# Kernel optimization log

Measured on AMD Instinct MI355X. Metric: run time of the kernel, lower is better.

Reference implementation:

```python
import jax, jax.numpy as jnp
import numpy as np

NUM_GROUPS, GROUP_SIZE, D_MODEL = 8, 4096, 1024
NUM_EXPERTS = 64
EXPERT_CAPACITY = 1024  # capacity_factor 2: 2 * total_tokens / num_experts


def setup_inputs() -> dict:
    key = jax.random.key(0)
    k1, k2, k3 = jax.random.split(key, 3)
    x = jax.random.normal(k1, (NUM_GROUPS, GROUP_SIZE, D_MODEL), dtype=jnp.float32)
    gate_kernel = jax.random.normal(k2, (D_MODEL, NUM_EXPERTS), dtype=jnp.float32) * 0.1
    gate_bias = jax.random.normal(k3, (NUM_EXPERTS,), dtype=jnp.float32) * 0.01
    temperature = jnp.ones((1,), dtype=jnp.float32)
    return {
        "x": x,
        "gate_kernel": gate_kernel,
        "gate_bias": gate_bias,
        "temperature": temperature,
        "expert_capacity": EXPERT_CAPACITY,
    }


def reference(x, gate_kernel, gate_bias, temperature, expert_capacity):
    # x: [G, S, D]; gate_kernel: [D, E]
    G, S, _ = x.shape
    E = gate_kernel.shape[1]

    router_logits = jnp.einsum("gsd,de->gse", x, gate_kernel) + gate_bias  # [G, S, E]
    safe_temp = jnp.maximum(temperature, 0.1)  # [1]
    router_probs = jax.nn.softmax(router_logits / safe_temp, axis=-1)  # [G, S, E]

    # Per-expert top-k over all flattened tokens.
    flat_probs = router_probs.transpose(2, 0, 1).reshape(E, G * S)  # [E, G*S]
    scores, token_indices = jax.lax.top_k(flat_probs, k=expert_capacity)  # [E, C]

    group_indices = token_indices // S  # [E, C]
    pos_indices = token_indices % S  # [E, C]
    expert_ids = jnp.broadcast_to(jnp.arange(E)[:, None], scores.shape)  # [E, C]

    # use_mask_routing=True path: scatter into capacity-limited dense masks.
    expert_masks = jnp.zeros((E, G, S), dtype=jnp.bool_).at[
        expert_ids, group_indices, pos_indices].set(True)
    weight_masks = jnp.zeros((E, G, S), dtype=x.dtype).at[
        expert_ids, group_indices, pos_indices].set(scores)

    loss = jnp.asarray(0.0, dtype=x.dtype)  # training=False
    return expert_masks, weight_masks, loss
```

## Files before the change

### kernel.cpp

```cpp
#include <hip/hip_runtime.h>
#include <math.h>

#define NG 8
#define SEQ 4096
#define DM 1024
#define NE 64
#define GS (NG * SEQ)
#define KSEL 1024
#define MASK_ELEMS (NE * GS)
#define SEG 16
#define SEGLEN (GS / SEG)
#define CAP 2048
#define CAP2 16384

typedef __attribute__((ext_vector_type(8))) short short8;
typedef __attribute__((ext_vector_type(4))) float f32x4;

__device__ __forceinline__ unsigned short f2bf(float v) {
  unsigned u = __float_as_uint(v);
  return (unsigned short)((u + 0x7FFFu + ((u >> 16) & 1u)) >> 16);
}
__device__ __forceinline__ float bf2f(unsigned short h) {
  return __uint_as_float(((unsigned)h) << 16);
}

#define GLDS(gsrc, ldst)                                                             \
  __builtin_amdgcn_global_load_lds(                                                  \
      (const __attribute__((address_space(1))) void*)(gsrc),                         \
      (__attribute__((address_space(3))) void*)(ldst), 16, 0, 0)

__global__ __launch_bounds__(256)
void k_split(const float* __restrict__ w, unsigned short* __restrict__ wph,
             unsigned short* __restrict__ wpm, unsigned* __restrict__ zbase) {
  const int t = blockIdx.x * 256 + threadIdx.x;
  if (t < NE * 256 + NE) zbase[t] = 0u;
  const int k = t >> 6, e = t & 63;
  float v = w[t];
  unsigned short h = f2bf(v); float r = v - bf2f(h);
  const int tile = k >> 5, g = (k >> 3) & 3, j = k & 7;
  const int cb = e >> 4, lrow = e & 15;
  const size_t o = (size_t)(tile * 4 + cb) * 512 + (g * 16 + lrow) * 8 + j;
  wph[o] = h; wpm[o] = f2bf(r);
}

__global__ __launch_bounds__(256, 2)
void k_gemm_softmax(const float* __restrict__ x,
                    const unsigned short* __restrict__ wph,
                    const unsigned short* __restrict__ wpm,
                    const float* __restrict__ bias, const float* __restrict__ temp,
                    float* __restrict__ probsT) {
  __shared__ float S[16384];
  float (*Pt)[68] = (float (*)[68])S;

  const int tid = threadIdx.x;
  const int w = tid >> 6, lane = tid & 63;
  const int lrow = lane & 15, g = lane >> 4;
  const int m0 = blockIdx.x * 64;
  const int ks0 = blockIdx.x & 15;
  const int arow_g = tid >> 4;
  const int agr = (tid & 15) ^ (arow_g & 15);

#define TS(u) (((u) + ks0) & 15)

  int irow[4], jcol[4];
  {
    union { unsigned short u[8]; short8 v; } ar, on;
#pragma unroll
    for (int j = 0; j < 8; ++j) { ar.u[j] = f2bf((float)lrow); on.u[j] = 0x3F80u; }
    f32x4 z = {0.f, 0.f, 0.f, 0.f};
    f32x4 p1 = __builtin_amdgcn_mfma_f32_16x16x32_bf16(ar.v, on.v, z, 0, 0, 0);
    f32x4 p2 = __builtin_amdgcn_mfma_f32_16x16x32_bf16(on.v, ar.v, z, 0, 0, 0);
#pragma unroll
    for (int b = 0; b < 4; ++b) {
      irow[b] = ((int)p1[b]) >> 5;
      jcol[b] = ((int)p2[b]) >> 5;
    }
  }

  f32x4 acc[4];
#pragma unroll
  for (int cb = 0; cb < 4; ++cb) acc[cb] = (f32x4){0.f, 0.f, 0.f, 0.f};

#define ISSUE(s, buf)                                                                \
  {                                                                                  \
    _Pragma("unroll")                                                                \
    for (int c = 0; c < 4; ++c)                                                      \
      GLDS(x + (size_t)(m0 + c * 16 + arow_g) * DM + (s) * 64 + agr * 4,             \
           S + (buf) * 8192 + (c * 256 + tid) * 4);                                  \
    _Pragma("unroll")                                                                \
    for (int p = 0; p < 2; ++p)                                                      \
      _Pragma("unroll")                                                              \
      for (int c = 0; c < 2; ++c)                                                    \
        GLDS((p ? wpm : wph) + (size_t)(s) * 4096 + c * 2048 + tid * 8,              \
             S + (buf) * 8192 + 4096 + p * 2048 + c * 1024 + tid * 4);               \
  }

#define COMPUTE(buf)                                                                 \
  {                                                                                  \
    const float* Af = S + (buf) * 8192;                                              \
    const unsigned short* Bb = (const unsigned short*)(S + (buf) * 8192 + 4096);     \
    _Pragma("unroll")                                                                \
    for (int kt = 0; kt < 2; ++kt) {                                                 \
      f32x4 lo = *(const f32x4*)(Af + (w * 16 + lrow) * 64 +                         \
                                 ((kt * 8 + g * 2 + 0) ^ lrow) * 4);                 \
      f32x4 hi = *(const f32x4*)(Af + (w * 16 + lrow) * 64 +                         \
                                 ((kt * 8 + g * 2 + 1) ^ lrow) * 4);                 \
      union { unsigned short u[8]; short8 v; } ah, am;                               \
      _Pragma("unroll")                                                              \
      for (int j = 0; j < 8; ++j) {                                                  \
        float v0 = (j < 4) ? lo[j] : hi[j - 4];                                      \
        unsigned short h_ = f2bf(v0);                                                \
        ah.u[j] = h_; am.u[j] = f2bf(v0 - bf2f(h_));                                 \
      }                                                                              \
      _Pragma("unroll")                                                              \
      for (int cb = 0; cb < 4; ++cb) {                                               \
        short8 bh_ = *(const short8*)(Bb + (kt * 4 + cb) * 512 + lane * 8);          \
        short8 bm_ = *(const short8*)(Bb + 4096 + (kt * 4 + cb) * 512 + lane * 8);   \
        acc[cb] = __builtin_amdgcn_mfma_f32_16x16x32_bf16(ah.v, bh_, acc[cb], 0, 0, 0); \
        acc[cb] = __builtin_amdgcn_mfma_f32_16x16x32_bf16(am.v, bh_, acc[cb], 0, 0, 0); \
        acc[cb] = __builtin_amdgcn_mfma_f32_16x16x32_bf16(ah.v, bm_, acc[cb], 0, 0, 0); \
      }                                                                              \
    }                                                                                \
  }

#define WAIT8 { asm volatile("s_waitcnt vmcnt(8)" ::: "memory");                     \
                __builtin_amdgcn_sched_barrier(0); }
#define WAIT0 { asm volatile("s_waitcnt vmcnt(0)" ::: "memory");                     \
                __builtin_amdgcn_sched_barrier(0); }

  ISSUE(TS(0), 0);
  ISSUE(TS(1), 1);
#pragma unroll
  for (int s = 0; s < 14; ++s) {
    WAIT8;
    __builtin_amdgcn_s_barrier();
    if (s & 1) { COMPUTE(1); } else { COMPUTE(0); }
    __builtin_amdgcn_s_barrier();
    ISSUE(TS(s + 2), s & 1);
  }
  WAIT8; __builtin_amdgcn_s_barrier(); COMPUTE(0);
  __builtin_amdgcn_s_barrier();
  WAIT0; __builtin_amdgcn_s_barrier(); COMPUTE(1);
  __syncthreads();

#undef ISSUE
#undef COMPUTE
#undef WAIT8
#undef WAIT0
#undef TS

  {
    float st = temp[0];
    if (st < 0.1f) st = 0.1f;
    const float inv_t = 1.0f / st;
#pragma unroll
    for (int b = 0; b < 4; ++b) {
      float l[4];
      float mx = -1.0e30f;
#pragma unroll
      for (int cb = 0; cb < 4; ++cb) {
        l[cb] = (acc[cb][b] + bias[cb * 16 + jcol[b]]) * inv_t;
        mx = fmaxf(mx, l[cb]);
      }
      mx = fmaxf(mx, __shfl_xor(mx, 1));
      mx = fmaxf(mx, __shfl_xor(mx, 2));
      mx = fmaxf(mx, __shfl_xor(mx, 4));
      mx = fmaxf(mx, __shfl_xor(mx, 8));
      float p[4], sm = 0.0f;
#pragma unroll
      for (int cb = 0; cb < 4; ++cb) { p[cb] = __expf(l[cb] - mx); sm += p[cb]; }
      sm += __shfl_xor(sm, 1);
      sm += __shfl_xor(sm, 2);
      sm += __shfl_xor(sm, 4);
      sm += __shfl_xor(sm, 8);
      const float invs = 1.0f / sm;
#pragma unroll
      for (int cb = 0; cb < 4; ++cb)
        Pt[cb * 16 + jcol[b]][w * 16 + irow[b]] = p[cb] * invs;
    }
  }
  __syncthreads();

  {
    const int e = tid >> 2, qq = tid & 3;
    float* dst = probsT + (size_t)e * GS + m0 + qq * 16;
#pragma unroll
    for (int c2 = 0; c2 < 4; ++c2)
      *(float4*)(dst + c2 * 4) = *(const float4*)(&Pt[e][qq * 16 + c2 * 4]);
  }
}

__device__ __forceinline__ void pick_scan(const unsigned* __restrict__ bins,
                                          unsigned r_in, unsigned& bucket,
                                          unsigned& r_out, unsigned* res) {
  __syncthreads();
  const int tid = threadIdx.x;
  if (tid < 64) {
    uint4 b = ((const uint4*)bins)[tid];
    unsigned s3 = b.w, s2 = b.z + s3, s1 = b.y + s2, s0 = b.x + s1;
    unsigned suf = s0;
#pragma unroll
    for (int off = 1; off < 64; off <<= 1) {
      unsigned t = __shfl_down(suf, off);
      if (tid + off < 64) suf += t;
    }
    unsigned above = suf - s0;
    unsigned inc0 = above + s0, inc1 = above + s1, inc2 = above + s2, inc3 = above + s3;
    if (inc3 >= r_in && inc3 - b.w < r_in) { res[0] = 4 * tid + 3; res[1] = r_in - (inc3 - b.w); }
    if (inc2 >= r_in && inc2 - b.z < r_in) { res[0] = 4 * tid + 2; res[1] = r_in - (inc2 - b.z); }
    if (inc1 >= r_in && inc1 - b.y < r_in) { res[0] = 4 * tid + 1; res[1] = r_in - (inc1 - b.y); }
    if (inc0 >= r_in && inc0 - b.x < r_in) { res[0] = 4 * tid + 0; res[1] = r_in - (inc0 - b.x); }
  }
  __syncthreads();
  bucket = res[0];
  r_out = res[1];
}

__global__ __launch_bounds__(256)
void k_hist0(const float* __restrict__ probsT, unsigned* __restrict__ ghist0) {
  __shared__ unsigned h[4][256];
  const int tid = threadIdx.x, wv = tid >> 6;
  const int e = blockIdx.x >> 4;
  const int seg = blockIdx.x & (SEG - 1);
  h[0][tid] = 0; h[1][tid] = 0; h[2][tid] = 0; h[3][tid] = 0;
  __syncthreads();
  const float4* col = (const float4*)(probsT + (size_t)e * GS + seg * SEGLEN);
#pragma unroll
  for (int i = 0; i < SEGLEN / 1024; ++i) {
    float4 v = col[i * 256 + tid];
    atomicAdd(&h[wv][__float_as_uint(v.x) >> 24], 1u);
    atomicAdd(&h[wv][__float_as_uint(v.y) >> 24], 1u);
    atomicAdd(&h[wv][__float_as_uint(v.z) >> 24], 1u);
    atomicAdd(&h[wv][__float_as_uint(v.w) >> 24], 1u);
  }
  __syncthreads();
  unsigned c = h[0][tid] + h[1][tid] + h[2][tid] + h[3][tid];
  if (c) atomicAdd(&ghist0[e * 256 + tid], c);
}

__global__ __launch_bounds__(256)
void k_compact(const float* __restrict__ probsT, const unsigned* __restrict__ ghist0,
               unsigned* __restrict__ cCnt, int* __restrict__ cIdx,
               float* __restrict__ cKey) {
  __shared__ unsigned res[2];
  __shared__ unsigned locN, basePos;
  __shared__ int locIdx[2048];
  __shared__ float locKey[2048];
  const int tid = threadIdx.x;
  const int e = blockIdx.x >> 4;
  const int seg = blockIdx.x & (SEG - 1);

  if (tid == 0) locN = 0u;
  unsigned b0, r0;
  pick_scan(ghist0 + e * 256, KSEL, b0, r0, res);
  const unsigned blo = (b0 == 0u) ? 0u : (b0 - 1u);

  const float* col = probsT + (size_t)e * GS + seg * SEGLEN;
  for (int i = 0; i < SEGLEN / 256; ++i) {
    const int t = i * 256 + tid;
    const float p = col[t];
    if ((__float_as_uint(p) >> 24) >= blo) {
      unsigned pos = atomicAdd(&locN, 1u);
      locIdx[pos] = seg * SEGLEN + t;
      locKey[pos] = p;
    }
  }
  __syncthreads();
  if (tid == 0) basePos = locN ? atomicAdd(&cCnt[e], locN) : 0u;
  __syncthreads();
  const unsigned n = locN, bp = basePos;
  for (unsigned i = tid; i < n; i += 256) {
    const unsigned gp = bp + i;
    if (gp < CAP2) {
      cIdx[(size_t)e * CAP2 + gp] = locIdx[i];
      cKey[(size_t)e * CAP2 + gp] = locKey[i];
    }
  }
}

__global__ __launch_bounds__(256)
void k_select2(const unsigned* __restrict__ ghist0, const unsigned* __restrict__ cCnt,
               const int* __restrict__ cIdx, const float* __restrict__ cKey,
               const float* __restrict__ temp, unsigned* __restrict__ defCnt,
               unsigned* __restrict__ candCnt, int* __restrict__ candIdx,
               float* __restrict__ thrHiA) {
  __shared__ unsigned res[2];
  __shared__ unsigned h[4][256];
  __shared__ unsigned hs[256];
  __shared__ unsigned nd, nc;
  const int tid = threadIdx.x, wv = tid >> 6;
  const int e = blockIdx.x;
  const int cnt = (int)min(cCnt[e], (unsigned)CAP2);

  unsigned b0, r;
  pick_scan(ghist0 + e * 256, KSEL, b0, r, res);
  unsigned pfx = b0 << 24;

  for (int pass = 1; pass < 4; ++pass) {
    const int shift = 24 - 8 * pass;
    const unsigned hm = 0xFFFFFFFFu << (shift + 8);
    for (int i = tid; i < 1024; i += 256) ((unsigned*)h)[i] = 0u;
    __syncthreads();
    for (int i = tid; i < cnt; i += 256) {
      unsigned key = __float_as_uint(cKey[(size_t)e * CAP2 + i]);
      if ((key & hm) == (pfx & hm)) atomicAdd(&h[wv][(key >> shift) & 255], 1u);
    }
    __syncthreads();
    hs[tid] = h[0][tid] + h[1][tid] + h[2][tid] + h[3][tid];
    unsigned b, rn;
    pick_scan(hs, r, b, rn, res);
    pfx |= b << shift;
    r = rn;
  }

  const float thrv = __uint_as_float(pfx);
  float st = temp[0];
  if (st < 0.1f) st = 0.1f;
  const float rel = 2.0e-3f / st;
  const float hi = thrv * (1.0f + rel);
  const float lo = thrv * (1.0f - rel);
  if (tid == 0) thrHiA[e] = hi;

  if (tid == 0) { nd = 0u; nc = 0u; }
  __syncthreads();
  for (int i = tid; i < cnt; i += 256) {
    const float p = cKey[(size_t)e * CAP2 + i];
    const int t = cIdx[(size_t)e * CAP2 + i];
    if (p > hi) {
      atomicAdd(&nd, 1u);
    } else if (p >= lo) {
      unsigned pos = atomicAdd(&nc, 1u);
      if (pos < CAP) candIdx[e * CAP + pos] = t;
    }
  }
  __syncthreads();
  if (tid == 0) {
    defCnt[e] = nd;
    candCnt[e] = min(nc, (unsigned)CAP);
  }
}

__global__ __launch_bounds__(256)
void k_repair(const float* __restrict__ x, const float* __restrict__ w,
              const float* __restrict__ bias, const float* __restrict__ temp,
              const unsigned* __restrict__ candCnt, const int* __restrict__ candIdx,
              double* __restrict__ candKey) {
  __shared__ double red[4][64];
  const int e = blockIdx.x >> 4;
  const int chunk = blockIdx.x & 15;
  const int tid = threadIdx.x;
  const int ee = tid & 63, q = tid >> 6;
  const int cnt = (int)min(candCnt[e], (unsigned)CAP);

  double st = (double)temp[0];
  if (st < 0.1) st = 0.1;
  const double inv_t = 1.0 / st;

  for (int i = chunk; i < cnt; i += 16) {
    const int t = candIdx[e * CAP + i];
    const float* xr = x + (size_t)t * DM;
    double s0 = 0.0, s1 = 0.0, s2 = 0.0, s3 = 0.0;
    const int kb = q * 256;
    for (int k = kb; k < kb + 256; k += 4) {
      s0 += (double)xr[k + 0] * (double)w[(size_t)(k + 0) * NE + ee];
      s1 += (double)xr[k + 1] * (double)w[(size_t)(k + 1) * NE + ee];
      s2 += (double)xr[k + 2] * (double)w[(size_t)(k + 2) * NE + ee];
      s3 += (double)xr[k + 3] * (double)w[(size_t)(k + 3) * NE + ee];
    }
    red[q][ee] = (s0 + s1) + (s2 + s3);
    __syncthreads();
    if (tid < 64) {
      double l = (red[0][tid] + red[1][tid] + red[2][tid] + red[3][tid] +
                  (double)bias[tid]) * inv_t;
      double m = l;
#pragma unroll
      for (int off = 1; off < 64; off <<= 1) m = fmax(m, __shfl_xor(m, off));
      double ex = exp(l - m);
      double ss = ex;
#pragma unroll
      for (int off = 1; off < 64; off <<= 1) ss += __shfl_xor(ss, off);
      if (tid == e) candKey[e * CAP + i] = ex / ss;
    }
    __syncthreads();
  }
}

__global__ __launch_bounds__(256)
void k_scatter(const float* __restrict__ probsT, const float* __restrict__ thrHiA,
               float* __restrict__ out) {
  const int gid = blockIdx.x * 256 + threadIdx.x;
  const int base = gid * 4;
  const int e = base >> 15;
  float4 p = *(const float4*)(probsT + (size_t)base);
  const float hi = thrHiA[e];
  float pv[4] = {p.x, p.y, p.z, p.w};
  float mk[4], wt[4];
#pragma unroll
  for (int c = 0; c < 4; ++c) {
    bool sel = pv[c] > hi;
    mk[c] = sel ? 1.0f : 0.0f;
    wt[c] = sel ? pv[c] : 0.0f;
  }
  *(float4*)(out + (size_t)base) = make_float4(mk[0], mk[1], mk[2], mk[3]);
  *(float4*)(out + (size_t)MASK_ELEMS + base) = make_float4(wt[0], wt[1], wt[2], wt[3]);
  if (gid == 0) out[2 * (size_t)MASK_ELEMS] = 0.0f;
}

__global__ __launch_bounds__(256)
void k_finish(const unsigned* __restrict__ defCnt, const unsigned* __restrict__ candCnt,
              const int* __restrict__ candIdx, const double* __restrict__ candKey,
              const float* __restrict__ probsT, float* __restrict__ out) {
  __shared__ double kd[CAP];
  __shared__ int ti[CAP];
  const int e = blockIdx.x, tid = threadIdx.x;
  const int cnt = (int)min(candCnt[e], (unsigned)CAP);
  const int need = KSEL - (int)defCnt[e];

  for (int i = tid; i < cnt; i += 256) {
    kd[i] = candKey[e * CAP + i];
    ti[i] = candIdx[e * CAP + i];
  }
  __syncthreads();
  for (int i = tid; i < cnt; i += 256) {
    const double ki = kd[i];
    const int tii = ti[i];
    int rank = 0;
    for (int j = 0; j < cnt; ++j)
      rank += (kd[j] > ki) || (kd[j] == ki && ti[j] < tii);
    if (rank < need) {
      out[(size_t)e * GS + tii] = 1.0f;
      out[(size_t)MASK_ELEMS + (size_t)e * GS + tii] = probsT[(size_t)e * GS + tii];
    }
  }
}

extern "C" void kernel_launch(void* const* d_in, const int* in_sizes, int n_in,
                              void* d_out, int out_size, void* d_ws, size_t ws_size,
                              hipStream_t stream) {
  const float* x    = (const float*)d_in[0];
  const float* gw   = (const float*)d_in[1];
  const float* gb   = (const float*)d_in[2];
  const float* temp = (const float*)d_in[3];

  float* probsT    = (float*)d_ws;
  unsigned* ghist0 = (unsigned*)((char*)d_ws + (size_t)MASK_ELEMS * 4);
  unsigned* cCnt   = ghist0 + NE * 256;
  unsigned* defCnt = cCnt + NE;
  unsigned* candCnt = defCnt + NE;
  float* thrHiA    = (float*)(candCnt + NE);
  int* candIdx     = (int*)(thrHiA + NE);
  double* candKey  = (double*)(candIdx + NE * CAP);
  int* cIdx        = (int*)(candKey + NE * CAP);
  float* cKey      = (float*)(cIdx + (size_t)NE * CAP2);
  unsigned short* wph = (unsigned short*)(cKey + (size_t)NE * CAP2);
  unsigned short* wpm = wph + DM * NE;

  k_split<<<DM * NE / 256, 256, 0, stream>>>(gw, wph, wpm, ghist0);
  k_gemm_softmax<<<GS / 64, 256, 0, stream>>>(x, wph, wpm, gb, temp, probsT);
  k_hist0<<<NE * SEG, 256, 0, stream>>>(probsT, ghist0);
  k_compact<<<NE * SEG, 256, 0, stream>>>(probsT, ghist0, cCnt, cIdx, cKey);
  k_select2<<<NE, 256, 0, stream>>>(ghist0, cCnt, cIdx, cKey, temp, defCnt,
                                    candCnt, candIdx, thrHiA);
  k_repair<<<NE * 16, 256, 0, stream>>>(x, gw, gb, temp, candCnt, candIdx, candKey);
  k_scatter<<<MASK_ELEMS / 1024, 256, 0, stream>>>(probsT, thrHiA, (float*)d_out);
  k_finish<<<NE, 256, 0, stream>>>(defCnt, candCnt, candIdx, candKey,
                                   probsT, (float*)d_out);
}
```

Baseline: 92.47 us.

## Fuse top-byte histogram into GEMM-softmax and deepen load pipeline to four stages

Removes the separate k_hist0 kernel. The GEMM-softmax kernel now builds a per-block 64x256 top-byte histogram in shared memory and atomically adds it to the global histogram, which avoids re-reading the full probsT array. The K-loop is also restructured into 32-wide K steps with a 4-deep ring buffer and vmcnt(12) waits. This deepens the prefetch, but the waits become finer-grained. The trade-off is extra block-level work: a 16K-entry LDS zero-fill and flush loop, plus many global atomics from every one of the 512 blocks.

```diff
diff --git a/kernel.cpp b/kernel.cpp
--- a/kernel.cpp
+++ b/kernel.cpp
@@ -48,19 +48,18 @@
                     const unsigned short* __restrict__ wph,
                     const unsigned short* __restrict__ wpm,
                     const float* __restrict__ bias, const float* __restrict__ temp,
-                    float* __restrict__ probsT) {
+                    float* __restrict__ probsT, unsigned* __restrict__ ghist0) {
   __shared__ float S[16384];
+  unsigned* Su = (unsigned*)S;
   float (*Pt)[68] = (float (*)[68])S;
 
   const int tid = threadIdx.x;
   const int w = tid >> 6, lane = tid & 63;
   const int lrow = lane & 15, g = lane >> 4;
   const int m0 = blockIdx.x * 64;
-  const int ks0 = blockIdx.x & 15;
-  const int arow_g = tid >> 4;
-  const int agr = (tid & 15) ^ (arow_g & 15);
-
-#define TS(u) (((u) + ks0) & 15)
+  const int ks0 = blockIdx.x & 31;
+
+#define TS(u) (((u) + ks0) & 31)
 
   int irow[4], jcol[4];
   {
@@ -84,71 +83,72 @@
 #define ISSUE(s, buf)                                                                \
   {                                                                                  \
     _Pragma("unroll")                                                                \
-    for (int c = 0; c < 4; ++c)                                                      \
-      GLDS(x + (size_t)(m0 + c * 16 + arow_g) * DM + (s) * 64 + agr * 4,             \
-           S + (buf) * 8192 + (c * 256 + tid) * 4);                                  \
+    for (int c = 0; c < 2; ++c) {                                                    \
+      const int idx = c * 256 + tid;                                                 \
+      const int row = idx >> 3, kg = (idx & 7) ^ (row & 7);                          \
+      GLDS(x + (size_t)(m0 + row) * DM + (s) * 32 + kg * 4,                          \
+           S + (buf) * 4096 + idx * 4);                                              \
+    }                                                                                \
     _Pragma("unroll")                                                                \
-    for (int p = 0; p < 2; ++p)                                                      \
-      _Pragma("unroll")                                                              \
-      for (int c = 0; c < 2; ++c)                                                    \
-        GLDS((p ? wpm : wph) + (size_t)(s) * 4096 + c * 2048 + tid * 8,              \
-             S + (buf) * 8192 + 4096 + p * 2048 + c * 1024 + tid * 4);               \
+    for (int c = 0; c < 2; ++c) {                                                    \
+      const int idx = c * 256 + tid;                                                 \
+      const unsigned short* bp = (idx >> 8) ? wpm : wph;                             \
+      GLDS(bp + (size_t)(s) * 2048 + (idx & 255) * 8,                                \
+           S + (buf) * 4096 + 2048 + idx * 4);                                       \
+    }                                                                                \
   }
 
 #define COMPUTE(buf)                                                                 \
   {                                                                                  \
-    const float* Af = S + (buf) * 8192;                                              \
-    const unsigned short* Bb = (const unsigned short*)(S + (buf) * 8192 + 4096);     \
+    const float* Af = S + (buf) * 4096;                                              \
+    const unsigned short* Bb = (const unsigned short*)(S + (buf) * 4096 + 2048);     \
+    const int row = w * 16 + lrow;                                                   \
+    f32x4 lo = *(const f32x4*)(Af + row * 32 + ((g * 2 + 0) ^ (row & 7)) * 4);       \
+    f32x4 hi = *(const f32x4*)(Af + row * 32 + ((g * 2 + 1) ^ (row & 7)) * 4);       \
+    union { unsigned short u[8]; short8 v; } ah, am;                                 \
     _Pragma("unroll")                                                                \
-    for (int kt = 0; kt < 2; ++kt) {                                                 \
-      f32x4 lo = *(const f32x4*)(Af + (w * 16 + lrow) * 64 +                         \
-                                 ((kt * 8 + g * 2 + 0) ^ lrow) * 4);                 \
-      f32x4 hi = *(const f32x4*)(Af + (w * 16 + lrow) * 64 +                         \
-                                 ((kt * 8 + g * 2 + 1) ^ lrow) * 4);                 \
-      union { unsigned short u[8]; short8 v; } ah, am;                               \
-      _Pragma("unroll")                                                              \
-      for (int j = 0; j < 8; ++j) {                                                  \
-        float v0 = (j < 4) ? lo[j] : hi[j - 4];                                      \
-        unsigned short h_ = f2bf(v0);                                                \
-        ah.u[j] = h_; am.u[j] = f2bf(v0 - bf2f(h_));                                 \
-      }                                                                              \
-      _Pragma("unroll")                                                              \
-      for (int cb = 0; cb < 4; ++cb) {                                               \
-        short8 bh_ = *(const short8*)(Bb + (kt * 4 + cb) * 512 + lane * 8);          \
-        short8 bm_ = *(const short8*)(Bb + 4096 + (kt * 4 + cb) * 512 + lane * 8);   \
-        acc[cb] = __builtin_amdgcn_mfma_f32_16x16x32_bf16(ah.v, bh_, acc[cb], 0, 0, 0); \
-        acc[cb] = __builtin_amdgcn_mfma_f32_16x16x32_bf16(am.v, bh_, acc[cb], 0, 0, 0); \
-        acc[cb] = __builtin_amdgcn_mfma_f32_16x16x32_bf16(ah.v, bm_, acc[cb], 0, 0, 0); \
-      }                                                                              \
+    for (int j = 0; j < 8; ++j) {                                                    \
+      float v0 = (j < 4) ? lo[j] : hi[j - 4];                                        \
+      unsigned short h_ = f2bf(v0);                                                  \
+      ah.u[j] = h_; am.u[j] = f2bf(v0 - bf2f(h_));                                   \
     }                                                                                \
-  }
-
-#define WAIT8 { asm volatile("s_waitcnt vmcnt(8)" ::: "memory");                     \
-                __builtin_amdgcn_sched_barrier(0); }
-#define WAIT0 { asm volatile("s_waitcnt vmcnt(0)" ::: "memory");                     \
-                __builtin_amdgcn_sched_barrier(0); }
+    _Pragma("unroll")                                                                \
+    for (int cb = 0; cb < 4; ++cb) {                                                 \
+      short8 bh_ = *(const short8*)(Bb + cb * 512 + lane * 8);                       \
+      short8 bm_ = *(const short8*)(Bb + 2048 + cb * 512 + lane * 8);                \
+      acc[cb] = __builtin_amdgcn_mfma_f32_16x16x32_bf16(ah.v, bh_, acc[cb], 0, 0, 0);\
+      acc[cb] = __builtin_amdgcn_mfma_f32_16x16x32_bf16(am.v, bh_, acc[cb], 0, 0, 0);\
+      acc[cb] = __builtin_amdgcn_mfma_f32_16x16x32_bf16(ah.v, bm_, acc[cb], 0, 0, 0);\
+    }                                                                                \
+  }
+
+#define WAITN(n) { asm volatile("s_waitcnt vmcnt(" #n ")" ::: "memory");             \
+                   __builtin_amdgcn_sched_barrier(0); }
 
   ISSUE(TS(0), 0);
   ISSUE(TS(1), 1);
-#pragma unroll
-  for (int s = 0; s < 14; ++s) {
-    WAIT8;
+  ISSUE(TS(2), 2);
+  ISSUE(TS(3), 3);
+#pragma unroll
+  for (int s = 0; s < 28; ++s) {
+    WAITN(12);
     __builtin_amdgcn_s_barrier();
-    if (s & 1) { COMPUTE(1); } else { COMPUTE(0); }
+    COMPUTE(s & 3);
     __builtin_amdgcn_s_barrier();
-    ISSUE(TS(s + 2), s & 1);
-  }
-  WAIT8; __builtin_amdgcn_s_barrier(); COMPUTE(0);
-  __builtin_amdgcn_s_barrier();
-  WAIT0; __builtin_amdgcn_s_barrier(); COMPUTE(1);
+    ISSUE(TS(s + 4), s & 3);
+  }
+  WAITN(12); __builtin_amdgcn_s_barrier(); COMPUTE(0);
+  WAITN(8);  __builtin_amdgcn_s_barrier(); COMPUTE(1);
+  WAITN(4);  __builtin_amdgcn_s_barrier(); COMPUTE(2);
+  WAITN(0);  __builtin_amdgcn_s_barrier(); COMPUTE(3);
   __syncthreads();
 
 #undef ISSUE
 #undef COMPUTE
-#undef WAIT8
-#undef WAIT0
+#undef WAITN
 #undef TS
 
+  float pn[4][4];
   {
     float st = temp[0];
     if (st < 0.1f) st = 0.1f;
@@ -175,12 +175,32 @@
       sm += __shfl_xor(sm, 8);
       const float invs = 1.0f / sm;
 #pragma unroll
-      for (int cb = 0; cb < 4; ++cb)
-        Pt[cb * 16 + jcol[b]][w * 16 + irow[b]] = p[cb] * invs;
-    }
-  }
-  __syncthreads();
-
+      for (int cb = 0; cb < 4; ++cb) pn[b][cb] = p[cb] * invs;
+    }
+  }
+
+  for (int i = tid; i < 16384; i += 256) Su[i] = 0u;
+  __syncthreads();
+#pragma unroll
+  for (int b = 0; b < 4; ++b)
+#pragma unroll
+    for (int cb = 0; cb < 4; ++cb) {
+      const int e = cb * 16 + jcol[b];
+      atomicAdd(&Su[e * 256 + (__float_as_uint(pn[b][cb]) >> 24)], 1u);
+    }
+  __syncthreads();
+  for (int i = tid; i < 16384; i += 256) {
+    const unsigned h = Su[i];
+    if (h) atomicAdd(&ghist0[i], h);
+  }
+  __syncthreads();
+
+#pragma unroll
+  for (int b = 0; b < 4; ++b)
+#pragma unroll
+    for (int cb = 0; cb < 4; ++cb)
+      Pt[cb * 16 + jcol[b]][w * 16 + irow[b]] = pn[b][cb];
+  __syncthreads();
   {
     const int e = tid >> 2, qq = tid & 3;
     float* dst = probsT + (size_t)e * GS + m0 + qq * 16;
@@ -214,28 +234,6 @@
   __syncthreads();
   bucket = res[0];
   r_out = res[1];
-}
-
-__global__ __launch_bounds__(256)
-void k_hist0(const float* __restrict__ probsT, unsigned* __restrict__ ghist0) {
-  __shared__ unsigned h[4][256];
-  const int tid = threadIdx.x, wv = tid >> 6;
-  const int e = blockIdx.x >> 4;
-  const int seg = blockIdx.x & (SEG - 1);
-  h[0][tid] = 0; h[1][tid] = 0; h[2][tid] = 0; h[3][tid] = 0;
-  __syncthreads();
-  const float4* col = (const float4*)(probsT + (size_t)e * GS + seg * SEGLEN);
-#pragma unroll
-  for (int i = 0; i < SEGLEN / 1024; ++i) {
-    float4 v = col[i * 256 + tid];
-    atomicAdd(&h[wv][__float_as_uint(v.x) >> 24], 1u);
-    atomicAdd(&h[wv][__float_as_uint(v.y) >> 24], 1u);
-    atomicAdd(&h[wv][__float_as_uint(v.z) >> 24], 1u);
-    atomicAdd(&h[wv][__float_as_uint(v.w) >> 24], 1u);
-  }
-  __syncthreads();
-  unsigned c = h[0][tid] + h[1][tid] + h[2][tid] + h[3][tid];
-  if (c) atomicAdd(&ghist0[e * 256 + tid], c);
 }
 
 __global__ __launch_bounds__(256)
@@ -456,8 +454,8 @@
   unsigned short* wpm = wph + DM * NE;
 
   k_split<<<DM * NE / 256, 256, 0, stream>>>(gw, wph, wpm, ghist0);
-  k_gemm_softmax<<<GS / 64, 256, 0, stream>>>(x, wph, wpm, gb, temp, probsT);
-  k_hist0<<<NE * SEG, 256, 0, stream>>>(probsT, ghist0);
+  k_gemm_softmax<<<GS / 64, 256, 0, stream>>>(x, wph, wpm, gb, temp, probsT,
+                                              ghist0);
   k_compact<<<NE * SEG, 256, 0, stream>>>(probsT, ghist0, cCnt, cIdx, cKey);
   k_select2<<<NE, 256, 0, stream>>>(ghist0, cCnt, cIdx, cKey, temp, defCnt,
                                     candCnt, candIdx, thrHiA);
```

New measurement: 100.5 us. +8.7%, slower.
